# Performance work log

Hardware: AMD Instinct MI355X
Metric: run time of the kernel (lower is better)

## Reference

```python
import jax, jax.numpy as jnp
import numpy as np


def _ln(x, g, b, eps=1e-5):
    mu = jnp.mean(x, axis=-1, keepdims=True)
    var = jnp.mean((x - mu) ** 2, axis=-1, keepdims=True)
    return (x - mu) * jax.lax.rsqrt(var + eps) * g + b


def setup_inputs() -> dict:
    key = jax.random.key(0)
    ks = jax.random.split(key, 12)
    B, H, W, D = 16, 128, 128, 64
    N = H * W
    Dff = 4 * D
    s = 0.02
    f32 = jnp.float32
    return {
        "x": jax.random.normal(ks[0], (B, N, D), f32),
        "H": H,
        "W": W,
        "ln1_scale": jnp.ones((D,), f32),
        "ln1_bias": jnp.zeros((D,), f32),
        "Wk": jax.random.normal(ks[1], (D, D), f32) * s,
        "bk": jnp.zeros((D,), f32),
        "Wq": jax.random.normal(ks[2], (D, D), f32) * s,
        "bq": jnp.zeros((D,), f32),
        "Wv": jax.random.normal(ks[3], (D, D), f32) * s,
        "bv": jnp.zeros((D,), f32),
        "Wr": jax.random.normal(ks[4], (D, D), f32) * s,
        "br": jnp.zeros((D,), f32),
        "ln2_scale": jnp.ones((D,), f32),
        "ln2_bias": jnp.zeros((D,), f32),
        "W1": jax.random.normal(ks[5], (Dff, D), f32) * s,
        "b1": jnp.zeros((Dff,), f32),
        "dw_w": jax.random.normal(ks[6], (Dff, 1, 3, 3), f32) * s,
        "dw_b": jnp.zeros((Dff,), f32),
        "W2": jax.random.normal(ks[7], (D, Dff), f32) * s,
        "b2": jnp.zeros((D,), f32),
    }


def reference(x, H, W, ln1_scale, ln1_bias, Wk, bk, Wq, bq, Wv, bv, Wr, br,
              ln2_scale, ln2_bias, W1, b1, dw_w, dw_b, W2, b2):
    B, N, D = x.shape
    Dff = W1.shape[0]

    # ---- EfficientAttention (head_count=1), tokens kept as [B, N, C] ----
    n1 = _ln(x, ln1_scale, ln1_bias)
    # 1x1 convs on [B,D,H,W] == per-token linear projections
    k = jax.nn.softmax(n1 @ Wk.T + bk, axis=1)    # softmax over spatial dim N (torch dim=2 of [B,Ck,N])
    q = jax.nn.softmax(n1 @ Wq.T + bq, axis=-1)   # softmax over key channels (torch dim=1)
    v = n1 @ Wv.T + bv                            # [B,N,Cv]
    context = jnp.einsum('bnk,bnv->bkv', k, v)    # key @ value^T, tiny [B,Ck,Cv]
    att = jnp.einsum('bkv,bnk->bnv', context, q)  # context^T @ query -> [B,N,Cv]
    attn_out = att @ Wr.T + br                    # reprojection 1x1 conv
    tx = x + attn_out

    # ---- MixFFN: fc1 -> depthwise 3x3 -> GELU -> fc2 ----
    n2 = _ln(tx, ln2_scale, ln2_bias)
    h = n2 @ W1.T + b1                            # [B,N,Dff]
    himg = jnp.transpose(h, (0, 2, 1)).reshape(B, Dff, H, W)
    conv = jax.lax.conv_general_dilated(
        himg, dw_w, window_strides=(1, 1), padding='SAME',
        feature_group_count=Dff,
        dimension_numbers=('NCHW', 'OIHW', 'NCHW')) + dw_b[None, :, None, None]
    h2 = jnp.transpose(conv.reshape(B, Dff, N), (0, 2, 1))
    h2 = jax.nn.gelu(h2, approximate=False)       # torch nn.GELU default is exact erf
    out = tx + (h2 @ W2.T + b2)
    return out
```

## Files before the change

kernel.cpp:

```cpp
#include <hip/hip_runtime.h>
#include <math.h>

typedef __bf16 bf16x8 __attribute__((ext_vector_type(8)));
typedef float f32x4 __attribute__((ext_vector_type(4)));
typedef float f32x2 __attribute__((ext_vector_type(2)));
typedef unsigned short u16x8 __attribute__((ext_vector_type(8)));
typedef unsigned short u16x4v __attribute__((ext_vector_type(4)));

constexpr int NIMG = 16384;
constexpr int HPITCH = 130;
constexpr int HROW = HPITCH*256;

__device__ __forceinline__ unsigned short f2bf(float f){
  unsigned u = __builtin_bit_cast(unsigned, f);
  u += 0x7fffu + ((u>>16)&1u);
  return (unsigned short)(u>>16);
}
__device__ __forceinline__ unsigned pack2(float a, float b){
  return (unsigned)f2bf(a) | ((unsigned)f2bf(b)<<16);
}
__device__ __forceinline__ float bf2f(unsigned short h){
  unsigned u = ((unsigned)h)<<16;
  return __builtin_bit_cast(float, u);
}
__device__ __forceinline__ bf16x8 ldfrag_g(const unsigned short* p){
  u16x8 v = *reinterpret_cast<const u16x8*>(p);
  return __builtin_bit_cast(bf16x8, v);
}
__device__ __forceinline__ f32x4 mfma16(bf16x8 a, bf16x8 b, f32x4 c){
  return __builtin_amdgcn_mfma_f32_16x16x32_bf16(a, b, c, 0, 0, 0);
}


__global__ __launch_bounds__(64) void k0_wfrag(
  const float* __restrict__ Wk, const float* __restrict__ Wq,
  const float* __restrict__ Wv, const float* __restrict__ Wr,
  const float* __restrict__ W1, const float* __restrict__ W2,
  const float* __restrict__ dww, const float* __restrict__ dwb,
  float* __restrict__ dwp, unsigned short* __restrict__ wf)
{
  const int bid = blockIdx.x, l = threadIdx.x;
  if (bid == 96){
    #pragma unroll
    for (int c=0;c<4;++c){
      int cp = l*4 + c;
      int f = ((cp&15)<<4) | (cp>>4);
      #pragma unroll
      for (int j=0;j<9;++j) dwp[cp*12 + j] = dww[f*9+j];
      dwp[cp*12 + 9]  = dwb[f];
      dwp[cp*12 + 10] = 0.f;
      dwp[cp*12 + 11] = 0.f;
    }
    return;
  }
  const float* src; int K, nt, ks; unsigned short* dst; bool perm = false;
  if (bid < 32){
    int w = bid>>3, f = bid&7;
    src = (w==0)?Wk:(w==1)?Wq:(w==2)?Wv:Wr;
    K = 64; nt = f>>1; ks = f&1;
    dst = wf + w*4096 + f*512;
  } else if (bid < 64){
    int f = bid-32; src = W1; K = 64; nt = f>>1; ks = f&1;
    dst = wf + 16384 + f*512;
  } else {
    int f = bid-64; src = W2; K = 256; nt = f>>3; ks = f&7;
    dst = wf + 32768 + f*512; perm = true;
  }
  u16x8 v;
  #pragma unroll
  for (int j=0;j<8;++j){
    int k = ks*32 + (l>>4)*8 + j;
    if (perm) k = ((k&15)<<4) | (k>>4);
    int n = nt*16 + (l&15);
    v[j] = f2bf(src[n*K + k]);
  }
  *reinterpret_cast<u16x8*>(dst + l*8) = v;
}

__global__ __launch_bounds__(256) void zhalo(unsigned* __restrict__ gh, unsigned* __restrict__ zr){
  int idx = blockIdx.x*256 + threadIdx.x;
  if (idx < 524288){
    int ch2 = idx & 127;
    int pos = idx >> 7;
    int side = pos & 1, row = pos >> 1;
    gh[(size_t)(row*HPITCH + side*(HPITCH-1))*128 + ch2] = 0;
  } else {
    int j = idx - 524288;
    if (j < HROW/2) zr[j] = 0;
  }
}

__global__ __launch_bounds__(256,2) void k1_ctx(
  const float* __restrict__ x, const float* __restrict__ g1, const float* __restrict__ be1,
  const float* __restrict__ bk, const float* __restrict__ bv,
  const unsigned short* __restrict__ wf,
  float* __restrict__ g_part, float* __restrict__ g_sump)
{
  __shared__ unsigned short tiles[4][4096];
  __shared__ float ctx_l[64*68];
  __shared__ float ssum_l[4][64];
  const int t = threadIdx.x, wid = t>>6, l = t&63;
  const int lg = l>>4, l15 = l&15;
  unsigned short* tile = tiles[wid];
  const int tok0 = blockIdx.x*512 + wid*128;

  bf16x8 WkF[8], WvF[8];
  #pragma unroll
  for (int f=0; f<8; ++f){
    WkF[f] = ldfrag_g(wf +    0 + f*512 + l*8);
    WvF[f] = ldfrag_g(wf + 8192 + f*512 + l*8);
  }
  float4 g1v  = *reinterpret_cast<const float4*>(&g1[l15*4]);
  float4 be1v = *reinterpret_cast<const float4*>(&be1[l15*4]);
  float bkv[4], bvv[4];
  #pragma unroll
  for (int ct=0; ct<4; ++ct){ bkv[ct]=bk[ct*16+l15]; bvv[ct]=bv[ct*16+l15]; }

  f32x4 acc[4][4];
  #pragma unroll
  for (int a=0;a<4;++a)
    #pragma unroll
    for (int b=0;b<4;++b) acc[a][b] = (f32x4){0.f,0.f,0.f,0.f};
  float sume[4] = {0.f,0.f,0.f,0.f};

  for (int tb=0; tb<2; ++tb){
    const int tbase = tok0 + tb*64;
    #pragma unroll
    for (int it=0; it<16; ++it){
      int row = it*4 + lg;
      float4 xv = *reinterpret_cast<const float4*>(&x[(size_t)(tbase+row)*64 + l15*4]);
      float s1 = xv.x+xv.y+xv.z+xv.w;
      float s2 = xv.x*xv.x + xv.y*xv.y + xv.z*xv.z + xv.w*xv.w;
      #pragma unroll
      for (int off=1; off<16; off<<=1){ s1 += __shfl_xor(s1,off,64); s2 += __shfl_xor(s2,off,64); }
      float mu = s1*(1.f/64.f);
      float rs = rsqrtf(s2*(1.f/64.f) - mu*mu + 1e-5f);
      uint2 pk = { pack2((xv.x-mu)*rs*g1v.x + be1v.x, (xv.y-mu)*rs*g1v.y + be1v.y),
                   pack2((xv.z-mu)*rs*g1v.z + be1v.z, (xv.w-mu)*rs*g1v.w + be1v.w) };
      *reinterpret_cast<uint2*>(&tile[row*64 + ((l15*4) ^ ((row&7)<<3))]) = pk;
    }
    bf16x8 aF[4][2];
    #pragma unroll
    for (int mt=0;mt<4;++mt){
      int row = mt*16+l15, sw=(row&7)<<3, ab=row*64;
      aF[mt][0] = __builtin_bit_cast(bf16x8, *reinterpret_cast<const u16x8*>(tile+ab+((     lg*8)^sw)));
      aF[mt][1] = __builtin_bit_cast(bf16x8, *reinterpret_cast<const u16x8*>(tile+ab+((32 + lg*8)^sw)));
    }
    #pragma unroll
    for (int half=0; half<2; ++half){
      #pragma unroll
      for (int m2=0;m2<2;++m2){
        const int mt = half*2+m2;
        #pragma unroll
        for (int ct=0;ct<4;++ct){
          f32x4 z = {0.f,0.f,0.f,0.f};
          z = mfma16(aF[mt][0], WkF[ct*2+0], z);
          z = mfma16(aF[mt][1], WkF[ct*2+1], z);
          float e0=__expf(z[0]+bkv[ct]), e1=__expf(z[1]+bkv[ct]);
          float e2=__expf(z[2]+bkv[ct]), e3=__expf(z[3]+bkv[ct]);
          sume[ct] += (e0+e1)+(e2+e3);
          const int c = ct*16+l15, sw = (c&7)<<3;
          const int cb = m2*16+lg*4;
          uint2 pe = { pack2(e0,e1), pack2(e2,e3) };
          *reinterpret_cast<uint2*>(&tile[c*64 + (cb ^ sw)]) = pe;
          f32x4 w = {0.f,0.f,0.f,0.f};
          w = mfma16(aF[mt][0], WvF[ct*2+0], w);
          w = mfma16(aF[mt][1], WvF[ct*2+1], w);
          uint2 pv = { pack2(w[0]+bvv[ct], w[1]+bvv[ct]), pack2(w[2]+bvv[ct], w[3]+bvv[ct]) };
          *reinterpret_cast<uint2*>(&tile[c*64 + ((32+cb) ^ sw)]) = pv;
        }
      }
      bf16x8 eA[4], vB[4];
      #pragma unroll
      for (int cm=0;cm<4;++cm){
        int row = cm*16+l15, sw=(row&7)<<3;
        eA[cm] = __builtin_bit_cast(bf16x8, *reinterpret_cast<const u16x8*>(tile + row*64 + ((     lg*8)^sw)));
        vB[cm] = __builtin_bit_cast(bf16x8, *reinterpret_cast<const u16x8*>(tile + row*64 + ((32 + lg*8)^sw)));
      }
      #pragma unroll
      for (int cm=0; cm<4; ++cm)
        #pragma unroll
        for (int jn=0; jn<4; ++jn)
          acc[cm][jn] = mfma16(eA[cm], vB[jn], acc[cm][jn]);
    }
  }
  #pragma unroll
  for (int ct=0; ct<4; ++ct){
    float s = sume[ct];
    s += __shfl_xor(s,16,64); s += __shfl_xor(s,32,64);
    if (lg==0) ssum_l[wid][ct*16+l15] = s;
  }
  #define CTX_RED(OP) \
    _Pragma("unroll") for (int cm=0;cm<4;++cm) \
    _Pragma("unroll") for (int jn=0;jn<4;++jn) \
    _Pragma("unroll") for (int r=0;r<4;++r) \
      ctx_l[(cm*16+lg*4+r)*68 + jn*16+l15] OP acc[cm][jn][r];
  if (wid==0){ CTX_RED(=) }  __syncthreads();
  if (wid==1){ CTX_RED(+=) } __syncthreads();
  if (wid==2){ CTX_RED(+=) } __syncthreads();
  if (wid==3){ CTX_RED(+=) } __syncthreads();
  #undef CTX_RED
  for (int i=t; i<4096; i+=256)
    g_part[(size_t)blockIdx.x*4096 + i] = ctx_l[(i>>6)*68 + (i&63)];
  if (t<64)
    g_sump[blockIdx.x*64 + t] = ssum_l[0][t]+ssum_l[1][t]+ssum_l[2][t]+ssum_l[3][t];
}

__global__ __launch_bounds__(512) void k15_ctxwr(
  const float* __restrict__ g_part, const float* __restrict__ g_sump,
  const float* __restrict__ Wr, unsigned short* __restrict__ ctxWrF)
{
  __shared__ float sctx[4096];
  __shared__ float sWr[4096];
  __shared__ float sinv[64];
  const int b = blockIdx.x, t = threadIdx.x;
  if (t<64){
    float s=0.f;
    #pragma unroll 8
    for (int p=0;p<32;++p) s += g_sump[(b*32+p)*64 + t];
    sinv[t] = 1.f/s;
  }
  for (int idx=t; idx<4096; idx+=512){
    float s=0.f;
    #pragma unroll 8
    for (int p=0;p<32;++p) s += g_part[(size_t)(b*32+p)*4096 + idx];
    sctx[idx] = s;
  }
  __syncthreads();
  {
    int c = t>>3, d0 = (t&7)*8;
    float invc = sinv[c];
    #pragma unroll
    for (int dd=0; dd<8; ++dd){
      int d = d0+dd; float s = 0.f;
      #pragma unroll
      for (int v=0; v<64; ++v) s += sctx[c*64+v]*Wr[d*64+v];
      sWr[c*64+d] = s*invc;
    }
  }
  __syncthreads();
  {
    int f = t>>6, l = t&63, nt = f>>1, ks = f&1;
    u16x8 v;
    #pragma unroll
    for (int j=0;j<8;++j){
      int k = ks*32 + (l>>4)*8 + j;
      int n = nt*16 + (l&15);
      v[j] = f2bf(sWr[k*64+n]);
    }
    *reinterpret_cast<u16x8*>(ctxWrF + b*4096 + f*512 + l*8) = v;
  }
}

__global__ __launch_bounds__(256,2) void k2_attn_ffn1(
  const float* __restrict__ x,
  const float* __restrict__ g1, const float* __restrict__ be1,
  const float* __restrict__ bq, const float* __restrict__ br,
  const float* __restrict__ g2, const float* __restrict__ be2,
  const float* __restrict__ b1,
  const unsigned short* __restrict__ wf,
  const unsigned short* __restrict__ ctxWrF,
  unsigned short* __restrict__ g_txb, unsigned short* __restrict__ g_h)
{
  __shared__ unsigned short tiles[4][4096];
  const int t = threadIdx.x, wid = t>>6, l = t&63;
  const int l15 = l&15, lg = l>>4;
  unsigned short* tile = tiles[wid];
  const int tok0 = (blockIdx.x*4 + wid)*64;
  const int img  = blockIdx.x>>6;
  const int yrow = (tok0>>7)&127;
  const int xb   = tok0&127;
  const size_t hbase = ((size_t)(img*128 + yrow)*HPITCH + 1 + xb)*256;

  bf16x8 WqF[8], CWF[8];
  #pragma unroll
  for (int f=0; f<8; ++f){
    WqF[f] = ldfrag_g(wf + 4096 + f*512 + l*8);
    CWF[f] = ldfrag_g(ctxWrF + img*4096 + f*512 + l*8);
  }
  float4 g1v  = *reinterpret_cast<const float4*>(&g1[l15*4]);
  float4 be1v = *reinterpret_cast<const float4*>(&be1[l15*4]);
  float bqv[4], brv[4], g2v[4], be2v[4];
  #pragma unroll
  for (int nt=0; nt<4; ++nt){
    bqv[nt]=bq[nt*16+l15]; brv[nt]=br[nt*16+l15];
    g2v[nt]=g2[nt*16+l15]; be2v[nt]=be2[nt*16+l15];
  }
  float b1v[16];
  #pragma unroll
  for (int i=0;i<16;++i) b1v[i]=b1[i*16+l15];

  #pragma unroll
  for (int it=0; it<16; ++it){
    int row = it*4 + lg;
    float4 xv = *reinterpret_cast<const float4*>(&x[(size_t)(tok0+row)*64 + l15*4]);
    float s1 = xv.x+xv.y+xv.z+xv.w;
    float s2 = xv.x*xv.x + xv.y*xv.y + xv.z*xv.z + xv.w*xv.w;
    #pragma unroll
    for (int off=1; off<16; off<<=1){ s1 += __shfl_xor(s1,off,64); s2 += __shfl_xor(s2,off,64); }
    float mu = s1*(1.f/64.f);
    float rs = rsqrtf(s2*(1.f/64.f) - mu*mu + 1e-5f);
    uint2 pk = { pack2((xv.x-mu)*rs*g1v.x + be1v.x, (xv.y-mu)*rs*g1v.y + be1v.y),
                 pack2((xv.z-mu)*rs*g1v.z + be1v.z, (xv.w-mu)*rs*g1v.w + be1v.w) };
    *reinterpret_cast<uint2*>(&tile[row*64 + ((l15*4) ^ ((row&7)<<3))]) = pk;
  }

  for (int mt=0; mt<4; ++mt){
    const int arow = mt*16 + l15;
    const int asw  = (arow&7)<<3;
    const int abase= arow*64;
    bf16x8 a0 = __builtin_bit_cast(bf16x8, *reinterpret_cast<const u16x8*>(tile + abase + ((     lg*8) ^ asw)));
    bf16x8 a1 = __builtin_bit_cast(bf16x8, *reinterpret_cast<const u16x8*>(tile + abase + ((32 + lg*8) ^ asw)));
    f32x4 qa[4];
    #pragma unroll
    for (int nt=0; nt<4; ++nt){
      f32x4 z = {0.f,0.f,0.f,0.f};
      z = mfma16(a0, WqF[nt*2+0], z);
      z = mfma16(a1, WqF[nt*2+1], z);
      qa[nt] = z;
    }
    #pragma unroll
    for (int nt=0; nt<4; ++nt)
      #pragma unroll
      for (int r=0; r<4; ++r) qa[nt][r] += bqv[nt];
    float mx[4];
    #pragma unroll
    for (int r=0;r<4;++r) mx[r] = fmaxf(fmaxf(qa[0][r],qa[1][r]), fmaxf(qa[2][r],qa[3][r]));
    #pragma unroll
    for (int off=1; off<16; off<<=1)
      #pragma unroll
      for (int r=0;r<4;++r) mx[r] = fmaxf(mx[r], __shfl_xor(mx[r], off, 64));
    float sm[4] = {0.f,0.f,0.f,0.f};
    #pragma unroll
    for (int nt=0;nt<4;++nt)
      #pragma unroll
      for (int r=0;r<4;++r){ float e = __expf(qa[nt][r]-mx[r]); qa[nt][r]=e; sm[r]+=e; }
    #pragma unroll
    for (int off=1; off<16; off<<=1)
      #pragma unroll
      for (int r=0;r<4;++r) sm[r] += __shfl_xor(sm[r], off, 64);
    float inv[4];
    #pragma unroll
    for (int r=0;r<4;++r) inv[r] = 1.f/sm[r];
    #pragma unroll
    for (int nt=0;nt<4;++nt)
      #pragma unroll
      for (int r=0;r<4;++r){
        int row = mt*16 + lg*4 + r, col = nt*16 + l15;
        tile[row*64 + (col ^ ((row&7)<<3))] = f2bf(qa[nt][r]*inv[r]);
      }
    bf16x8 p0 = __builtin_bit_cast(bf16x8, *reinterpret_cast<const u16x8*>(tile + abase + ((     lg*8) ^ asw)));
    bf16x8 p1 = __builtin_bit_cast(bf16x8, *reinterpret_cast<const u16x8*>(tile + abase + ((32 + lg*8) ^ asw)));
    f32x4 ao[4];
    #pragma unroll
    for (int nt=0; nt<4; ++nt){
      f32x4 z = {0.f,0.f,0.f,0.f};
      z = mfma16(p0, CWF[nt*2+0], z);
      z = mfma16(p1, CWF[nt*2+1], z);
      ao[nt] = z;
    }
    float txv[4][4];
    float s1v[4] = {0.f,0.f,0.f,0.f}, s2v[4] = {0.f,0.f,0.f,0.f};
    #pragma unroll
    for (int nt=0;nt<4;++nt)
      #pragma unroll
      for (int r=0;r<4;++r){
        size_t row = (size_t)(tok0 + mt*16 + lg*4 + r);
        float v = ao[nt][r] + brv[nt] + x[row*64 + nt*16+l15];
        g_txb[row*64 + nt*16+l15] = f2bf(v);
        txv[nt][r] = v; s1v[r] += v; s2v[r] += v*v;
      }
    #pragma unroll
    for (int off=1; off<16; off<<=1)
      #pragma unroll
      for (int r=0;r<4;++r){ s1v[r] += __shfl_xor(s1v[r], off, 64); s2v[r] += __shfl_xor(s2v[r], off, 64); }
    #pragma unroll
    for (int r=0;r<4;++r){
      float mu2 = s1v[r]*(1.f/64.f);
      float rs  = rsqrtf(s2v[r]*(1.f/64.f) - mu2*mu2 + 1e-5f);
      s1v[r] = mu2; s2v[r] = rs;
    }
    #pragma unroll
    for (int nt=0;nt<4;++nt)
      #pragma unroll
      for (int r=0;r<4;++r){
        int row = mt*16 + lg*4 + r, col = nt*16 + l15;
        float n2 = (txv[nt][r]-s1v[r])*s2v[r]*g2v[nt] + be2v[nt];
        tile[row*64 + (col ^ ((row&7)<<3))] = f2bf(n2);
      }
  }

  for (int mt=0; mt<4; ++mt){
    const int arow = mt*16 + l15;
    const int asw  = (arow&7)<<3;
    const int abase= arow*64;
    bf16x8 n20 = __builtin_bit_cast(bf16x8, *reinterpret_cast<const u16x8*>(tile + abase + ((     lg*8) ^ asw)));
    bf16x8 n21 = __builtin_bit_cast(bf16x8, *reinterpret_cast<const u16x8*>(tile + abase + ((32 + lg*8) ^ asw)));
    unsigned hpk[4][8];
    #pragma unroll
    for (int np=0; np<8; ++np){
      bf16x8 wa0 = ldfrag_g(wf + 16384 + (np*4+0)*512 + l*8);
      bf16x8 wa1 = ldfrag_g(wf + 16384 + (np*4+1)*512 + l*8);
      bf16x8 wb0 = ldfrag_g(wf + 16384 + (np*4+2)*512 + l*8);
      bf16x8 wb1 = ldfrag_g(wf + 16384 + (np*4+3)*512 + l*8);
      float ba = b1v[np*2], bb = b1v[np*2+1];
      f32x4 ha = {ba,ba,ba,ba};
      ha = mfma16(n20, wa0, ha);
      ha = mfma16(n21, wa1, ha);
      f32x4 hb = {bb,bb,bb,bb};
      hb = mfma16(n20, wb0, hb);
      hb = mfma16(n21, wb1, hb);
      #pragma unroll
      for (int r=0;r<4;++r) hpk[r][np] = pack2(ha[r], hb[r]);
    }
    #pragma unroll
    for (int r=0;r<4;++r){
      const size_t ro = hbase + (size_t)(mt*16+lg*4+r)*256 + l15*16;
      uint4 v0 = { hpk[r][0], hpk[r][1], hpk[r][2], hpk[r][3] };
      uint4 v1 = { hpk[r][4], hpk[r][5], hpk[r][6], hpk[r][7] };
      *reinterpret_cast<uint4*>(&g_h[ro])   = v0;
      *reinterpret_cast<uint4*>(&g_h[ro+8]) = v1;
    }
  }
}

__global__ __launch_bounds__(256,3) void k3_conv_ffn2(
  const unsigned short* __restrict__ g_h,
  const unsigned short* __restrict__ zrow,
  const float* __restrict__ dwp,
  const float* __restrict__ b2,
  const unsigned short* __restrict__ wf,
  const unsigned short* __restrict__ g_txb, float* __restrict__ out)
{
  __shared__ unsigned ring[4][2304];
  __shared__ unsigned short obuf[2][4096];
  const int t = threadIdx.x, w = t>>6, l = t&63;
  const int l15 = l&15, lg = l>>4;
  const int bid = (blockIdx.x & 7)*128 + (blockIdx.x >> 3);
  const int img = bid>>6;
  const int r6  = bid&63;
  const int y0  = (r6>>3)*16, x0 = (r6&7)*16;

  const float4 tA = *reinterpret_cast<const float4*>(&dwp[t*12]);
  const float4 tB = *reinterpret_cast<const float4*>(&dwp[t*12+4]);
  const float4 tC = *reinterpret_cast<const float4*>(&dwp[t*12+8]);

  bf16x8 W2F[8];
  #pragma unroll
  for (int q=0;q<8;++q)
    W2F[q] = ldfrag_g(wf + 32768 + (w*8 + q)*512 + l*8);
  const float4 b2q = *reinterpret_cast<const float4*>(&b2[w*16 + lg*4]);

  const int di = w*576 + l;

  auto rowsrc = [&](int ri) -> const unsigned* {
    return (ri>=0 && ri<128)
      ? reinterpret_cast<const unsigned*>(g_h + ((size_t)(img*128+ri)*HPITCH + x0)*256)
      : reinterpret_cast<const unsigned*>(zrow + x0*256);
  };

  {
    unsigned st[3][9];
    #pragma unroll
    for (int k=0;k<3;++k){
      const unsigned* src = rowsrc(y0-1+k);
      #pragma unroll
      for (int i=0;i<9;++i) st[k][i] = src[di + i*64];
    }
    #pragma unroll
    for (int k=0;k<3;++k)
      #pragma unroll
      for (int i=0;i<9;++i) ring[k][di + i*64] = st[k][i];
  }
  __syncthreads();

  for (int yy=0; yy<16; ++yy){
    const int gy = y0 + yy;
    unsigned rr[9];
    {
      const unsigned* src = rowsrc(gy+2);
      #pragma unroll
      for (int i=0;i<9;++i) rr[i] = src[di + i*64];
    }
    const size_t gtok = (size_t)img*16384 + (size_t)gy*128 + x0 + l15;
    const u16x4v tq = *reinterpret_cast<const u16x4v*>(&g_txb[gtok*64 + w*16 + lg*4]);

    const unsigned short* rA16 = reinterpret_cast<const unsigned short*>(ring[(yy  )&3]);
    const unsigned short* rB16 = reinterpret_cast<const unsigned short*>(ring[(yy+1)&3]);
    const unsigned short* rC16 = reinterpret_cast<const unsigned short*>(ring[(yy+2)&3]);
    unsigned short* ob = obuf[yy&1];

    float pA=bf2f(rA16[t]),     pB=bf2f(rB16[t]),     pC=bf2f(rC16[t]);
    float cA=bf2f(rA16[256+t]), cB=bf2f(rB16[256+t]), cC=bf2f(rC16[256+t]);
    unsigned short qA=rA16[512+t], qB=rB16[512+t], qC=rC16[512+t];
    #pragma unroll
    for (int s=0;s<16;++s){
      const int o = (s<15 ? (s+3) : 17)*256 + t;
      unsigned short zA=rA16[o], zB=rB16[o], zC=rC16[o];
      float nA=bf2f(qA), nB=bf2f(qB), nC=bf2f(qC);
      float a = tC.y;
      a = fmaf(tA.x,pA, a); a = fmaf(tA.y,cA, a); a = fmaf(tA.z,nA, a);
      a = fmaf(tA.w,pB, a); a = fmaf(tB.x,cB, a); a = fmaf(tB.y,nB, a);
      a = fmaf(tB.z,pC, a); a = fmaf(tB.w,cC, a); a = fmaf(tC.x,nC, a);
      float u2 = a*a;
      float arg = a*(-2.3022082f - 0.1029432f*u2);
      float e = __builtin_amdgcn_exp2f(arg);
      float g = a*__builtin_amdgcn_rcpf(1.f + e);
      ob[s*256 + (t ^ ((s&7)<<3))] = f2bf(g);
      pA=cA; pB=cB; pC=cC; cA=nA; cB=nB; cC=nC; qA=zA; qB=zB; qC=zC;
    }

    {
      unsigned* dstr = ring[(yy+3)&3];
      #pragma unroll
      for (int i=0;i<9;++i) dstr[di + i*64] = rr[i];
    }
    __syncthreads();

    f32x4 oacc = {0.f,0.f,0.f,0.f};
    const int nsw = (l15&7)<<3;
    #pragma unroll
    for (int i=0;i<4;++i){
      bf16x8 fb0 = __builtin_bit_cast(bf16x8,
        *reinterpret_cast<const u16x8*>(&ob[l15*256 + ((i*64      + lg*8) ^ nsw)]));
      bf16x8 fb1 = __builtin_bit_cast(bf16x8,
        *reinterpret_cast<const u16x8*>(&ob[l15*256 + ((i*64 + 32 + lg*8) ^ nsw)]));
      oacc = mfma16(W2F[i*2+0], fb0, oacc);
      oacc = mfma16(W2F[i*2+1], fb1, oacc);
    }
    float4 o;
    o.x = oacc[0] + b2q.x + bf2f(tq[0]);
    o.y = oacc[1] + b2q.y + bf2f(tq[1]);
    o.z = oacc[2] + b2q.z + bf2f(tq[2]);
    o.w = oacc[3] + b2q.w + bf2f(tq[3]);
    *reinterpret_cast<float4*>(&out[gtok*64 + w*16 + lg*4]) = o;
  }
}

extern "C" void kernel_launch(void* const* d_in, const int* in_sizes, int n_in,
                              void* d_out, int out_size, void* d_ws, size_t ws_size,
                              hipStream_t stream)
{
  const float* x  =(const float*)d_in[0];
  const float* g1 =(const float*)d_in[3];
  const float* be1=(const float*)d_in[4];
  const float* Wk =(const float*)d_in[5];
  const float* bk =(const float*)d_in[6];
  const float* Wq =(const float*)d_in[7];
  const float* bq =(const float*)d_in[8];
  const float* Wv =(const float*)d_in[9];
  const float* bv =(const float*)d_in[10];
  const float* Wr =(const float*)d_in[11];
  const float* br =(const float*)d_in[12];
  const float* g2 =(const float*)d_in[13];
  const float* be2=(const float*)d_in[14];
  const float* W1 =(const float*)d_in[15];
  const float* b1 =(const float*)d_in[16];
  const float* dww=(const float*)d_in[17];
  const float* dwb=(const float*)d_in[18];
  const float* W2 =(const float*)d_in[19];
  const float* b2 =(const float*)d_in[20];
  float* outp = (float*)d_out;
  char* ws = (char*)d_ws;

  unsigned short* wfb    = (unsigned short*)ws;
  unsigned short* ctxWrF = (unsigned short*)(ws + 98304);
  float* g_sump = (float*)(ws + 229376);
  float* g_part = (float*)(ws + 393216);
  unsigned short* g_txb = (unsigned short*)(ws + 16777216);
  unsigned short* g_h   = (unsigned short*)(ws + 50331648);
  unsigned short* zr    = (unsigned short*)(ws + 186646528);
  float* dwp            = (float*)(ws + 186712064);

  hipLaunchKernelGGL(k0_wfrag, dim3(97), dim3(64), 0, stream, Wk, Wq, Wv, Wr, W1, W2, dww, dwb, dwp, wfb);
  hipLaunchKernelGGL(zhalo, dim3(2113), dim3(256), 0, stream, (unsigned*)g_h, (unsigned*)zr);
  hipLaunchKernelGGL(k1_ctx, dim3(512), dim3(256), 0, stream, x, g1, be1, bk, bv, wfb, g_part, g_sump);
  hipLaunchKernelGGL(k15_ctxwr, dim3(16), dim3(512), 0, stream, g_part, g_sump, Wr, ctxWrF);
  hipLaunchKernelGGL(k2_attn_ffn1, dim3(1024), dim3(256), 0, stream,
                     x, g1, be1, bq, br, g2, be2, b1, wfb, ctxWrF, g_txb, g_h);
  hipLaunchKernelGGL(k3_conv_ffn2, dim3(1024), dim3(256), 0, stream,
                     g_h, zr, dwp, b2, wfb, g_txb, outp);
}
```

Before: 237.1 us.

## Move fc1 into conv kernel to avoid writing the 256-channel hidden tensor

k2 now writes only the 64-channel LayerNorm2 output (n2) in bf16 instead of the 256-channel fc1 result with halo padding. The conv/fc2 kernel recomputes fc1 per input row with MFMA from a staged n2 tile, including halo columns and rows, and writes the results into a swizzled LDS ring. This removes the zero-halo kernel and cuts the hidden-tensor global traffic by about 4x. In exchange, fc1 is recomputed for halo rows and columns (18/16 wide, rows shared via the ring), and occupancy drops from 3 to 2 blocks per CU.

```diff
diff --git a/kernel.cpp b/kernel.cpp
--- a/kernel.cpp
+++ b/kernel.cpp
@@ -3,13 +3,8 @@
 
 typedef __bf16 bf16x8 __attribute__((ext_vector_type(8)));
 typedef float f32x4 __attribute__((ext_vector_type(4)));
-typedef float f32x2 __attribute__((ext_vector_type(2)));
 typedef unsigned short u16x8 __attribute__((ext_vector_type(8)));
 typedef unsigned short u16x4v __attribute__((ext_vector_type(4)));
-
-constexpr int NIMG = 16384;
-constexpr int HPITCH = 130;
-constexpr int HROW = HPITCH*256;
 
 __device__ __forceinline__ unsigned short f2bf(float f){
   unsigned u = __builtin_bit_cast(unsigned, f);
@@ -75,19 +70,6 @@
     v[j] = f2bf(src[n*K + k]);
   }
   *reinterpret_cast<u16x8*>(dst + l*8) = v;
-}
-
-__global__ __launch_bounds__(256) void zhalo(unsigned* __restrict__ gh, unsigned* __restrict__ zr){
-  int idx = blockIdx.x*256 + threadIdx.x;
-  if (idx < 524288){
-    int ch2 = idx & 127;
-    int pos = idx >> 7;
-    int side = pos & 1, row = pos >> 1;
-    gh[(size_t)(row*HPITCH + side*(HPITCH-1))*128 + ch2] = 0;
-  } else {
-    int j = idx - 524288;
-    if (j < HROW/2) zr[j] = 0;
-  }
 }
 
 __global__ __launch_bounds__(256,2) void k1_ctx(
@@ -257,10 +239,9 @@
   const float* __restrict__ g1, const float* __restrict__ be1,
   const float* __restrict__ bq, const float* __restrict__ br,
   const float* __restrict__ g2, const float* __restrict__ be2,
-  const float* __restrict__ b1,
   const unsigned short* __restrict__ wf,
   const unsigned short* __restrict__ ctxWrF,
-  unsigned short* __restrict__ g_txb, unsigned short* __restrict__ g_h)
+  unsigned short* __restrict__ g_txb, unsigned short* __restrict__ n2g)
 {
   __shared__ unsigned short tiles[4][4096];
   const int t = threadIdx.x, wid = t>>6, l = t&63;
@@ -268,9 +249,6 @@
   unsigned short* tile = tiles[wid];
   const int tok0 = (blockIdx.x*4 + wid)*64;
   const int img  = blockIdx.x>>6;
-  const int yrow = (tok0>>7)&127;
-  const int xb   = tok0&127;
-  const size_t hbase = ((size_t)(img*128 + yrow)*HPITCH + 1 + xb)*256;
 
   bf16x8 WqF[8], CWF[8];
   #pragma unroll
@@ -286,9 +264,6 @@
     bqv[nt]=bq[nt*16+l15]; brv[nt]=br[nt*16+l15];
     g2v[nt]=g2[nt*16+l15]; be2v[nt]=be2[nt*16+l15];
   }
-  float b1v[16];
-  #pragma unroll
-  for (int i=0;i<16;++i) b1v[i]=b1[i*16+l15];
 
   #pragma unroll
   for (int it=0; it<16; ++it){
@@ -390,56 +365,32 @@
       }
   }
 
-  for (int mt=0; mt<4; ++mt){
-    const int arow = mt*16 + l15;
-    const int asw  = (arow&7)<<3;
-    const int abase= arow*64;
-    bf16x8 n20 = __builtin_bit_cast(bf16x8, *reinterpret_cast<const u16x8*>(tile + abase + ((     lg*8) ^ asw)));
-    bf16x8 n21 = __builtin_bit_cast(bf16x8, *reinterpret_cast<const u16x8*>(tile + abase + ((32 + lg*8) ^ asw)));
-    unsigned hpk[4][8];
-    #pragma unroll
-    for (int np=0; np<8; ++np){
-      bf16x8 wa0 = ldfrag_g(wf + 16384 + (np*4+0)*512 + l*8);
-      bf16x8 wa1 = ldfrag_g(wf + 16384 + (np*4+1)*512 + l*8);
-      bf16x8 wb0 = ldfrag_g(wf + 16384 + (np*4+2)*512 + l*8);
-      bf16x8 wb1 = ldfrag_g(wf + 16384 + (np*4+3)*512 + l*8);
-      float ba = b1v[np*2], bb = b1v[np*2+1];
-      f32x4 ha = {ba,ba,ba,ba};
-      ha = mfma16(n20, wa0, ha);
-      ha = mfma16(n21, wa1, ha);
-      f32x4 hb = {bb,bb,bb,bb};
-      hb = mfma16(n20, wb0, hb);
-      hb = mfma16(n21, wb1, hb);
-      #pragma unroll
-      for (int r=0;r<4;++r) hpk[r][np] = pack2(ha[r], hb[r]);
-    }
-    #pragma unroll
-    for (int r=0;r<4;++r){
-      const size_t ro = hbase + (size_t)(mt*16+lg*4+r)*256 + l15*16;
-      uint4 v0 = { hpk[r][0], hpk[r][1], hpk[r][2], hpk[r][3] };
-      uint4 v1 = { hpk[r][4], hpk[r][5], hpk[r][6], hpk[r][7] };
-      *reinterpret_cast<uint4*>(&g_h[ro])   = v0;
-      *reinterpret_cast<uint4*>(&g_h[ro+8]) = v1;
-    }
-  }
-}
-
-__global__ __launch_bounds__(256,3) void k3_conv_ffn2(
-  const unsigned short* __restrict__ g_h,
-  const unsigned short* __restrict__ zrow,
+  #pragma unroll
+  for (int c=0;c<8;++c){
+    int idx = c*64 + l;
+    int tok = idx>>3, b8 = (idx&7)*8;
+    u16x8 v = *reinterpret_cast<const u16x8*>(tile + tok*64 + (b8 ^ ((tok&7)<<3)));
+    *reinterpret_cast<u16x8*>(n2g + (size_t)(tok0+tok)*64 + b8) = v;
+  }
+}
+
+__global__ __launch_bounds__(256,2) void k3_conv_ffn2(
+  const unsigned short* __restrict__ n2g,
   const float* __restrict__ dwp,
+  const float* __restrict__ b1,
   const float* __restrict__ b2,
   const unsigned short* __restrict__ wf,
   const unsigned short* __restrict__ g_txb, float* __restrict__ out)
 {
-  __shared__ unsigned ring[4][2304];
+  __shared__ unsigned short ring[4][4608];
+  __shared__ unsigned short n2s[2][2048];
   __shared__ unsigned short obuf[2][4096];
   const int t = threadIdx.x, w = t>>6, l = t&63;
   const int l15 = l&15, lg = l>>4;
   const int bid = (blockIdx.x & 7)*128 + (blockIdx.x >> 3);
   const int img = bid>>6;
   const int r6  = bid&63;
-  const int y0  = (r6>>3)*16, x0 = (r6&7)*16;
+  const int y0  = (r6>>3)*16, xb = (r6&7)*16;
 
   const float4 tA = *reinterpret_cast<const float4*>(&dwp[t*12]);
   const float4 tB = *reinterpret_cast<const float4*>(&dwp[t*12+4]);
@@ -451,74 +402,112 @@
     W2F[q] = ldfrag_g(wf + 32768 + (w*8 + q)*512 + l*8);
   const float4 b2q = *reinterpret_cast<const float4*>(&b2[w*16 + lg*4]);
 
-  const int di = w*576 + l;
-
-  auto rowsrc = [&](int ri) -> const unsigned* {
-    return (ri>=0 && ri<128)
-      ? reinterpret_cast<const unsigned*>(g_h + ((size_t)(img*128+ri)*HPITCH + x0)*256)
-      : reinterpret_cast<const unsigned*>(zrow + x0*256);
+  float b1w[4];
+  #pragma unroll
+  for (int q=0;q<4;++q) b1w[q] = b1[(w*4+q)*16 + l15];
+
+  const int si = t>>3, sb = (t&7)*8;
+  const unsigned short* n2img = n2g + (size_t)img*16384*64;
+
+  auto ldstage = [&](int r, u16x8* v){
+    int rc = r < 0 ? 0 : (r > 127 ? 127 : r);
+    int xx = xb - 8 + si; xx = xx < 0 ? 0 : (xx > 127 ? 127 : xx);
+    *v = *reinterpret_cast<const u16x8*>(n2img + ((size_t)rc*128 + xx)*64 + sb);
   };
+  auto stwrite = [&](int buf, u16x8 v){
+    *reinterpret_cast<u16x8*>(&n2s[buf][si*64 + (sb ^ ((si&7)<<3))]) = v;
+  };
+  auto W1row = [&](int sl, int r, const unsigned short* ns){
+    const bool rv = (r >= 0 && r < 128);
+    bf16x8 a00, a01, a10, a11;
+    {
+      int tok = l15, sw = (tok&7)<<3, ab = tok*64;
+      a00 = __builtin_bit_cast(bf16x8, *reinterpret_cast<const u16x8*>(ns + ab + ((     lg*8)^sw)));
+      a01 = __builtin_bit_cast(bf16x8, *reinterpret_cast<const u16x8*>(ns + ab + ((32 + lg*8)^sw)));
+    }
+    {
+      int tok = 16 + l15, sw = (tok&7)<<3, ab = tok*64;
+      a10 = __builtin_bit_cast(bf16x8, *reinterpret_cast<const u16x8*>(ns + ab + ((     lg*8)^sw)));
+      a11 = __builtin_bit_cast(bf16x8, *reinterpret_cast<const u16x8*>(ns + ab + ((32 + lg*8)^sw)));
+    }
+    unsigned short* rg = ring[sl];
+    #pragma unroll
+    for (int q=0;q<4;++q){
+      const int nt2 = w*4 + q;
+      bf16x8 w0 = ldfrag_g(wf + 16384 + (nt2*2+0)*512 + l*8);
+      bf16x8 w1 = ldfrag_g(wf + 16384 + (nt2*2+1)*512 + l*8);
+      const int cp = l15*16 + nt2;
+      #pragma unroll
+      for (int mt2=0; mt2<2; ++mt2){
+        f32x4 h = {b1w[q], b1w[q], b1w[q], b1w[q]};
+        h = mfma16(mt2 ? a10 : a00, w0, h);
+        h = mfma16(mt2 ? a11 : a01, w1, h);
+        #pragma unroll
+        for (int r4=0; r4<4; ++r4){
+          int p = mt2*16 + lg*4 + r4 - 7;
+          if (p >= 0 && p < 18){
+            int xx = xb - 1 + p;
+            float v = (rv && xx >= 0 && xx < 128) ? h[r4] : 0.f;
+            rg[p*256 + (cp ^ ((p&3)<<4))] = f2bf(v);
+          }
+        }
+      }
+    }
+  };
 
   {
-    unsigned st[3][9];
-    #pragma unroll
-    for (int k=0;k<3;++k){
-      const unsigned* src = rowsrc(y0-1+k);
-      #pragma unroll
-      for (int i=0;i<9;++i) st[k][i] = src[di + i*64];
-    }
-    #pragma unroll
-    for (int k=0;k<3;++k)
-      #pragma unroll
-      for (int i=0;i<9;++i) ring[k][di + i*64] = st[k][i];
-  }
-  __syncthreads();
+    u16x8 sv;
+    ldstage(y0-1, &sv); stwrite(0, sv); __syncthreads();
+    W1row(0, y0-1, n2s[0]);
+    ldstage(y0, &sv); stwrite(1, sv); __syncthreads();
+    W1row(1, y0, n2s[1]);
+    ldstage(y0+1, &sv); stwrite(0, sv); __syncthreads();
+    W1row(2, y0+1, n2s[0]);
+    ldstage(y0+2, &sv); stwrite(1, sv); __syncthreads();
+  }
 
   for (int yy=0; yy<16; ++yy){
     const int gy = y0 + yy;
-    unsigned rr[9];
+    u16x8 sv;
+    if (yy < 15) ldstage(gy+3, &sv);
+    const size_t gtok = (size_t)img*16384 + (size_t)gy*128 + xb + l15;
+    const u16x4v tq = *reinterpret_cast<const u16x4v*>(&g_txb[gtok*64 + w*16 + lg*4]);
+
+    W1row((yy+3)&3, gy+2, n2s[(yy+1)&1]);
+
     {
-      const unsigned* src = rowsrc(gy+2);
-      #pragma unroll
-      for (int i=0;i<9;++i) rr[i] = src[di + i*64];
-    }
-    const size_t gtok = (size_t)img*16384 + (size_t)gy*128 + x0 + l15;
-    const u16x4v tq = *reinterpret_cast<const u16x4v*>(&g_txb[gtok*64 + w*16 + lg*4]);
-
-    const unsigned short* rA16 = reinterpret_cast<const unsigned short*>(ring[(yy  )&3]);
-    const unsigned short* rB16 = reinterpret_cast<const unsigned short*>(ring[(yy+1)&3]);
-    const unsigned short* rC16 = reinterpret_cast<const unsigned short*>(ring[(yy+2)&3]);
-    unsigned short* ob = obuf[yy&1];
-
-    float pA=bf2f(rA16[t]),     pB=bf2f(rB16[t]),     pC=bf2f(rC16[t]);
-    float cA=bf2f(rA16[256+t]), cB=bf2f(rB16[256+t]), cC=bf2f(rC16[256+t]);
-    unsigned short qA=rA16[512+t], qB=rB16[512+t], qC=rC16[512+t];
-    #pragma unroll
-    for (int s=0;s<16;++s){
-      const int o = (s<15 ? (s+3) : 17)*256 + t;
-      unsigned short zA=rA16[o], zB=rB16[o], zC=rC16[o];
-      float nA=bf2f(qA), nB=bf2f(qB), nC=bf2f(qC);
-      float a = tC.y;
-      a = fmaf(tA.x,pA, a); a = fmaf(tA.y,cA, a); a = fmaf(tA.z,nA, a);
-      a = fmaf(tA.w,pB, a); a = fmaf(tB.x,cB, a); a = fmaf(tB.y,nB, a);
-      a = fmaf(tB.z,pC, a); a = fmaf(tB.w,cC, a); a = fmaf(tC.x,nC, a);
-      float u2 = a*a;
-      float arg = a*(-2.3022082f - 0.1029432f*u2);
-      float e = __builtin_amdgcn_exp2f(arg);
-      float g = a*__builtin_amdgcn_rcpf(1.f + e);
-      ob[s*256 + (t ^ ((s&7)<<3))] = f2bf(g);
-      pA=cA; pB=cB; pC=cC; cA=nA; cB=nB; cC=nC; qA=zA; qB=zB; qC=zC;
-    }
-
-    {
-      unsigned* dstr = ring[(yy+3)&3];
-      #pragma unroll
-      for (int i=0;i<9;++i) dstr[di + i*64] = rr[i];
-    }
+      const unsigned short* rA16 = ring[(yy  )&3];
+      const unsigned short* rB16 = ring[(yy+1)&3];
+      const unsigned short* rC16 = ring[(yy+2)&3];
+      unsigned short* ob = obuf[yy&1];
+      const int c0 = t, c1 = t^16, c2 = t^32;
+      float pA=bf2f(rA16[c0]),      pB=bf2f(rB16[c0]),      pC=bf2f(rC16[c0]);
+      float cA=bf2f(rA16[256+c1]),  cB=bf2f(rB16[256+c1]),  cC=bf2f(rC16[256+c1]);
+      unsigned short qA=rA16[512+c2], qB=rB16[512+c2], qC=rC16[512+c2];
+      #pragma unroll
+      for (int s=0;s<16;++s){
+        const int oo = (s<15 ? s+3 : 17);
+        const int oc = oo*256 + (t ^ ((oo&3)<<4));
+        unsigned short zA=rA16[oc], zB=rB16[oc], zC=rC16[oc];
+        float nA=bf2f(qA), nB=bf2f(qB), nC=bf2f(qC);
+        float a = tC.y;
+        a = fmaf(tA.x,pA, a); a = fmaf(tA.y,cA, a); a = fmaf(tA.z,nA, a);
+        a = fmaf(tA.w,pB, a); a = fmaf(tB.x,cB, a); a = fmaf(tB.y,nB, a);
+        a = fmaf(tB.z,pC, a); a = fmaf(tB.w,cC, a); a = fmaf(tC.x,nC, a);
+        float u2 = a*a;
+        float arg = a*(-2.3022082f - 0.1029432f*u2);
+        float e = __builtin_amdgcn_exp2f(arg);
+        float g = a*__builtin_amdgcn_rcpf(1.f + e);
+        ob[s*256 + (t ^ ((s&7)<<3))] = f2bf(g);
+        pA=cA; pB=cB; pC=cC; cA=nA; cB=nB; cC=nC; qA=zA; qB=zB; qC=zC;
+      }
+    }
+    if (yy < 15) stwrite(yy&1, sv);
     __syncthreads();
 
     f32x4 oacc = {0.f,0.f,0.f,0.f};
     const int nsw = (l15&7)<<3;
+    const unsigned short* ob = obuf[yy&1];
     #pragma unroll
     for (int i=0;i<4;++i){
       bf16x8 fb0 = __builtin_bit_cast(bf16x8,
@@ -568,16 +557,14 @@
   float* g_sump = (float*)(ws + 229376);
   float* g_part = (float*)(ws + 393216);
   unsigned short* g_txb = (unsigned short*)(ws + 16777216);
-  unsigned short* g_h   = (unsigned short*)(ws + 50331648);
-  unsigned short* zr    = (unsigned short*)(ws + 186646528);
+  unsigned short* n2g   = (unsigned short*)(ws + 50331648);
   float* dwp            = (float*)(ws + 186712064);
 
   hipLaunchKernelGGL(k0_wfrag, dim3(97), dim3(64), 0, stream, Wk, Wq, Wv, Wr, W1, W2, dww, dwb, dwp, wfb);
-  hipLaunchKernelGGL(zhalo, dim3(2113), dim3(256), 0, stream, (unsigned*)g_h, (unsigned*)zr);
   hipLaunchKernelGGL(k1_ctx, dim3(512), dim3(256), 0, stream, x, g1, be1, bk, bv, wfb, g_part, g_sump);
   hipLaunchKernelGGL(k15_ctxwr, dim3(16), dim3(512), 0, stream, g_part, g_sump, Wr, ctxWrF);
   hipLaunchKernelGGL(k2_attn_ffn1, dim3(1024), dim3(256), 0, stream,
-                     x, g1, be1, bq, br, g2, be2, b1, wfb, ctxWrF, g_txb, g_h);
+                     x, g1, be1, bq, br, g2, be2, wfb, ctxWrF, g_txb, n2g);
   hipLaunchKernelGGL(k3_conv_ffn2, dim3(1024), dim3(256), 0, stream,
-                     g_h, zr, dwp, b2, wfb, g_txb, outp);
-}
+                     n2g, dwp, b1, b2, wfb, g_txb, outp);
+}
```

Result: slower. 256.7 us (+8.3%).

## Store FFN hidden activations as FP8 to halve intermediate traffic

Applied to the files above, without the earlier changes.

The fc1 output h is now packed to FP8 with hardware cvt_pk_fp8 instructions instead of bf16, halving the bytes written by k2 and read by k3 for the largest intermediate tensor. k3 loads FP8 rows, converts them back to bf16 when filling the shared-memory ring, and uses a padded ring pitch. The halo-zeroing kernel is resized to the new byte layout. This trades numerical precision of the hidden activations (e4m3/fp8 rounding) for lower memory bandwidth, plus extra conversion ALU work in k3.

```diff
diff --git a/kernel.cpp b/kernel.cpp
--- a/kernel.cpp
+++ b/kernel.cpp
@@ -9,7 +9,6 @@
 
 constexpr int NIMG = 16384;
 constexpr int HPITCH = 130;
-constexpr int HROW = HPITCH*256;
 
 __device__ __forceinline__ unsigned short f2bf(float f){
   unsigned u = __builtin_bit_cast(unsigned, f);
@@ -79,14 +78,14 @@
 
 __global__ __launch_bounds__(256) void zhalo(unsigned* __restrict__ gh, unsigned* __restrict__ zr){
   int idx = blockIdx.x*256 + threadIdx.x;
-  if (idx < 524288){
-    int ch2 = idx & 127;
-    int pos = idx >> 7;
+  if (idx < 262144){
+    int ch = idx & 63;
+    int pos = idx >> 6;
     int side = pos & 1, row = pos >> 1;
-    gh[(size_t)(row*HPITCH + side*(HPITCH-1))*128 + ch2] = 0;
+    gh[(size_t)(row*HPITCH + side*(HPITCH-1))*64 + ch] = 0;
   } else {
-    int j = idx - 524288;
-    if (j < HROW/2) zr[j] = 0;
+    int j = idx - 262144;
+    if (j < 8320) zr[j] = 0;
   }
 }
 
@@ -260,7 +259,7 @@
   const float* __restrict__ b1,
   const unsigned short* __restrict__ wf,
   const unsigned short* __restrict__ ctxWrF,
-  unsigned short* __restrict__ g_txb, unsigned short* __restrict__ g_h)
+  unsigned short* __restrict__ g_txb, unsigned char* __restrict__ g_h)
 {
   __shared__ unsigned short tiles[4][4096];
   const int t = threadIdx.x, wid = t>>6, l = t&63;
@@ -396,7 +395,7 @@
     const int abase= arow*64;
     bf16x8 n20 = __builtin_bit_cast(bf16x8, *reinterpret_cast<const u16x8*>(tile + abase + ((     lg*8) ^ asw)));
     bf16x8 n21 = __builtin_bit_cast(bf16x8, *reinterpret_cast<const u16x8*>(tile + abase + ((32 + lg*8) ^ asw)));
-    unsigned hpk[4][8];
+    unsigned hq[4][4];
     #pragma unroll
     for (int np=0; np<8; ++np){
       bf16x8 wa0 = ldfrag_g(wf + 16384 + (np*4+0)*512 + l*8);
@@ -410,29 +409,35 @@
       f32x4 hb = {bb,bb,bb,bb};
       hb = mfma16(n20, wb0, hb);
       hb = mfma16(n21, wb1, hb);
-      #pragma unroll
-      for (int r=0;r<4;++r) hpk[r][np] = pack2(ha[r], hb[r]);
+      const int d = np>>1;
+      if ((np&1)==0){
+        #pragma unroll
+        for (int r=0;r<4;++r)
+          hq[r][d] = (unsigned)__builtin_amdgcn_cvt_pk_fp8_f32(ha[r], hb[r], 0, false);
+      } else {
+        #pragma unroll
+        for (int r=0;r<4;++r)
+          hq[r][d] = (unsigned)__builtin_amdgcn_cvt_pk_fp8_f32(ha[r], hb[r], (int)hq[r][d], true);
+      }
     }
     #pragma unroll
     for (int r=0;r<4;++r){
       const size_t ro = hbase + (size_t)(mt*16+lg*4+r)*256 + l15*16;
-      uint4 v0 = { hpk[r][0], hpk[r][1], hpk[r][2], hpk[r][3] };
-      uint4 v1 = { hpk[r][4], hpk[r][5], hpk[r][6], hpk[r][7] };
-      *reinterpret_cast<uint4*>(&g_h[ro])   = v0;
-      *reinterpret_cast<uint4*>(&g_h[ro+8]) = v1;
+      uint4 v = { hq[r][0], hq[r][1], hq[r][2], hq[r][3] };
+      *reinterpret_cast<uint4*>(g_h + ro) = v;
     }
   }
 }
 
 __global__ __launch_bounds__(256,3) void k3_conv_ffn2(
-  const unsigned short* __restrict__ g_h,
-  const unsigned short* __restrict__ zrow,
+  const unsigned char* __restrict__ g_h,
+  const unsigned char* __restrict__ zrow,
   const float* __restrict__ dwp,
   const float* __restrict__ b2,
   const unsigned short* __restrict__ wf,
   const unsigned short* __restrict__ g_txb, float* __restrict__ out)
 {
-  __shared__ unsigned ring[4][2304];
+  __shared__ unsigned ring[4][2322];
   __shared__ unsigned short obuf[2][4096];
   const int t = threadIdx.x, w = t>>6, l = t&63;
   const int l15 = l&15, lg = l>>4;
@@ -451,37 +456,53 @@
     W2F[q] = ldfrag_g(wf + 32768 + (w*8 + q)*512 + l*8);
   const float4 b2q = *reinterpret_cast<const float4*>(&b2[w*16 + lg*4]);
 
-  const int di = w*576 + l;
-
-  auto rowsrc = [&](int ri) -> const unsigned* {
+  const int pi = 1 + (t&15);
+  const int c0 = (t>>4)*16;
+
+  auto rowsrc = [&](int ri) -> const unsigned char* {
     return (ri>=0 && ri<128)
-      ? reinterpret_cast<const unsigned*>(g_h + ((size_t)(img*128+ri)*HPITCH + x0)*256)
-      : reinterpret_cast<const unsigned*>(zrow + x0*256);
+      ? g_h + ((size_t)(img*128+ri)*HPITCH + x0)*256
+      : zrow + x0*256;
   };
+  auto ldrow = [&](int ri, uint4* m, unsigned* h){
+    const unsigned char* src = rowsrc(ri);
+    *m = *reinterpret_cast<const uint4*>(src + pi*256 + c0);
+    if (t < 128){
+      int ph = (t<64)?0:17, dh = t&63;
+      *h = reinterpret_cast<const unsigned*>(src + ph*256)[dh];
+    }
+  };
+  auto cvtwr = [&](unsigned* rg, int base, unsigned mdw){
+    f32x2 lo = __builtin_amdgcn_cvt_pk_f32_fp8((int)mdw, false);
+    f32x2 hi = __builtin_amdgcn_cvt_pk_f32_fp8((int)mdw, true);
+    unsigned plo, phi;
+    asm("v_cvt_pk_bf16_f32 %0, %1, %2" : "=v"(plo) : "v"(lo[0]), "v"(lo[1]));
+    asm("v_cvt_pk_bf16_f32 %0, %1, %2" : "=v"(phi) : "v"(hi[0]), "v"(hi[1]));
+    rg[base]   = plo;
+    rg[base+1] = phi;
+  };
+  auto wrrow = [&](int sl, uint4 m, unsigned h){
+    unsigned* rg = ring[sl];
+    const int base = pi*129 + (c0>>1);
+    #pragma unroll
+    for (int d=0; d<4; ++d) cvtwr(rg, base + 2*d, m[d]);
+    if (t < 128){
+      int ph = (t<64)?0:17, dh = t&63;
+      cvtwr(rg, ph*129 + 2*dh, h);
+    }
+  };
 
   {
-    unsigned st[3][9];
-    #pragma unroll
-    for (int k=0;k<3;++k){
-      const unsigned* src = rowsrc(y0-1+k);
-      #pragma unroll
-      for (int i=0;i<9;++i) st[k][i] = src[di + i*64];
-    }
-    #pragma unroll
-    for (int k=0;k<3;++k)
-      #pragma unroll
-      for (int i=0;i<9;++i) ring[k][di + i*64] = st[k][i];
+    uint4 m0,m1,m2; unsigned h0=0,h1=0,h2=0;
+    ldrow(y0-1,&m0,&h0); ldrow(y0,&m1,&h1); ldrow(y0+1,&m2,&h2);
+    wrrow(0,m0,h0); wrrow(1,m1,h1); wrrow(2,m2,h2);
   }
   __syncthreads();
 
   for (int yy=0; yy<16; ++yy){
     const int gy = y0 + yy;
-    unsigned rr[9];
-    {
-      const unsigned* src = rowsrc(gy+2);
-      #pragma unroll
-      for (int i=0;i<9;++i) rr[i] = src[di + i*64];
-    }
+    uint4 rm; unsigned rh = 0;
+    ldrow(gy+2, &rm, &rh);
     const size_t gtok = (size_t)img*16384 + (size_t)gy*128 + x0 + l15;
     const u16x4v tq = *reinterpret_cast<const u16x4v*>(&g_txb[gtok*64 + w*16 + lg*4]);
 
@@ -491,11 +512,11 @@
     unsigned short* ob = obuf[yy&1];
 
     float pA=bf2f(rA16[t]),     pB=bf2f(rB16[t]),     pC=bf2f(rC16[t]);
-    float cA=bf2f(rA16[256+t]), cB=bf2f(rB16[256+t]), cC=bf2f(rC16[256+t]);
-    unsigned short qA=rA16[512+t], qB=rB16[512+t], qC=rC16[512+t];
+    float cA=bf2f(rA16[258+t]), cB=bf2f(rB16[258+t]), cC=bf2f(rC16[258+t]);
+    unsigned short qA=rA16[516+t], qB=rB16[516+t], qC=rC16[516+t];
     #pragma unroll
     for (int s=0;s<16;++s){
-      const int o = (s<15 ? (s+3) : 17)*256 + t;
+      const int o = (s<15 ? (s+3) : 17)*258 + t;
       unsigned short zA=rA16[o], zB=rB16[o], zC=rC16[o];
       float nA=bf2f(qA), nB=bf2f(qB), nC=bf2f(qC);
       float a = tC.y;
@@ -510,11 +531,7 @@
       pA=cA; pB=cB; pC=cC; cA=nA; cB=nB; cC=nC; qA=zA; qB=zB; qC=zC;
     }
 
-    {
-      unsigned* dstr = ring[(yy+3)&3];
-      #pragma unroll
-      for (int i=0;i<9;++i) dstr[di + i*64] = rr[i];
-    }
+    wrrow((yy+3)&3, rm, rh);
     __syncthreads();
 
     f32x4 oacc = {0.f,0.f,0.f,0.f};
@@ -568,12 +585,12 @@
   float* g_sump = (float*)(ws + 229376);
   float* g_part = (float*)(ws + 393216);
   unsigned short* g_txb = (unsigned short*)(ws + 16777216);
-  unsigned short* g_h   = (unsigned short*)(ws + 50331648);
-  unsigned short* zr    = (unsigned short*)(ws + 186646528);
+  unsigned char* g_h    = (unsigned char*)(ws + 50331648);
+  unsigned char* zr     = (unsigned char*)(ws + 186646528);
   float* dwp            = (float*)(ws + 186712064);
 
   hipLaunchKernelGGL(k0_wfrag, dim3(97), dim3(64), 0, stream, Wk, Wq, Wv, Wr, W1, W2, dww, dwb, dwp, wfb);
-  hipLaunchKernelGGL(zhalo, dim3(2113), dim3(256), 0, stream, (unsigned*)g_h, (unsigned*)zr);
+  hipLaunchKernelGGL(zhalo, dim3(1057), dim3(256), 0, stream, (unsigned*)g_h, (unsigned*)zr);
   hipLaunchKernelGGL(k1_ctx, dim3(512), dim3(256), 0, stream, x, g1, be1, bk, bv, wfb, g_part, g_sump);
   hipLaunchKernelGGL(k15_ctxwr, dim3(16), dim3(512), 0, stream, g_part, g_sump, Wr, ctxWrF);
   hipLaunchKernelGGL(k2_attn_ffn1, dim3(1024), dim3(256), 0, stream,
```

Result: faster. 209.9 us (-11.5%).
